# Kernel optimization log

Hardware: AMD Instinct MI355X
Metric: run time of the kernel (lower is better)

## Reference

```python
import jax, jax.numpy as jnp
import numpy as np

N_PRED = 2_000_000   # predicted reflections (incl. harmonics)
N_OBS = 1_000_000    # merged observations (harmonic groups)
RASU = 200_000       # reciprocal ASU size
N_IMAGES = 2000
HMAX = 60
GRID = 2 * HMAX + 1  # 121
MC = 32              # mc_samples
D_META = 5
KL_WEIGHT = 1.0
LOG2PI = float(np.log(2.0 * np.pi))

# 3 reindexing ops as integer 3x3 matrices: identity, inversion, a permutation op
OPS = np.stack([
    np.eye(3, dtype=np.int32),
    -np.eye(3, dtype=np.int32),
    np.array([[0, 1, 0], [1, 0, 0], [0, 0, -1]], dtype=np.int32),
])


def setup_inputs() -> dict:
    key = jax.random.key(0)
    ks = jax.random.split(key, 12)
    hkl = jax.random.randint(ks[0], (N_PRED, 3), -HMAX, HMAX + 1, dtype=jnp.int32)
    asu_table = jax.random.randint(ks[1], (GRID ** 3,), 0, RASU, dtype=jnp.int32)
    harmonic_id = jnp.arange(N_PRED, dtype=jnp.int32) // 2  # 2 harmonics per obs, max = N_OBS-1
    image_id = jax.random.randint(ks[2], (N_PRED,), 0, N_IMAGES, dtype=jnp.int32)
    I = jax.random.normal(ks[3], (N_OBS,), dtype=jnp.float32)
    SigI = jax.random.uniform(ks[4], (N_OBS,), minval=0.5, maxval=1.5, dtype=jnp.float32)
    metadata = jax.random.normal(ks[5], (N_PRED, D_META), dtype=jnp.float32)
    q_loc = jax.random.normal(ks[6], (RASU,), dtype=jnp.float32)
    q_raw_scale = jax.random.normal(ks[7], (RASU,), dtype=jnp.float32) * 0.1
    eps = jax.random.normal(ks[8], (MC, RASU), dtype=jnp.float32)
    scale_w = jax.random.normal(ks[9], (D_META + 4,), dtype=jnp.float32) * 0.01
    scale_b = jnp.zeros((), dtype=jnp.float32)
    image_bias = jax.random.normal(ks[10], (N_IMAGES,), dtype=jnp.float32) * 0.01
    return dict(hkl=hkl, I=I, SigI=SigI, image_id=image_id, metadata=metadata,
                harmonic_id=harmonic_id, asu_table=asu_table, q_loc=q_loc,
                q_raw_scale=q_raw_scale, eps=eps, scale_w=scale_w, scale_b=scale_b,
                image_bias=image_bias)


def reference(hkl, I, SigI, image_id, metadata, harmonic_id, asu_table,
              q_loc, q_raw_scale, eps, scale_w, scale_b, image_bias):
    q_scale = jax.nn.softplus(q_raw_scale) + 1e-6
    # KL(q || N(0,1)) for Normal q, then mean over reflections
    kl_div = jnp.mean(-jnp.log(q_scale) + 0.5 * (q_scale ** 2 + q_loc ** 2) - 0.5)

    Imodel = jnp.stack([q_loc, q_scale], axis=-1)           # [RASU, 2]
    Iscale = jnp.stack([I, SigI], axis=-1)[harmonic_id]      # [N_PRED, 2] (gathered per prediction)
    zT = (q_loc[None, :] + q_scale[None, :] * eps).T         # rsample -> [RASU, MC]

    log_sig = jnp.log(SigI)[:, None]
    lls = []
    for op in OPS:  # small fixed loop over reindexing ops
        _hkl = hkl @ jnp.asarray(op).T                       # [N_PRED, 3]
        flat = ((_hkl[:, 0] + HMAX) * GRID + (_hkl[:, 1] + HMAX)) * GRID + (_hkl[:, 2] + HMAX)
        refl_id = asu_table[flat]                            # reciprocal_asu lookup [N_PRED]
        feats = jnp.concatenate([Imodel[refl_id], Iscale, metadata], axis=-1)  # [N_PRED, 9]
        scale = jnp.exp(feats @ scale_w + scale_b + image_bias[image_id])[:, None]
        Ipred = zT[refl_id] * scale                          # [N_PRED, MC]
        # convolve: scatter-add harmonics into observations
        Ipred = jax.ops.segment_sum(Ipred, harmonic_id, num_segments=N_OBS)  # [N_OBS, MC]
        ll = -0.5 * ((Ipred - I[:, None]) / SigI[:, None]) ** 2 - log_sig - 0.5 * LOG2PI
        # build per-observation image id (default 1, overwritten by scatter)
        img_obs = jnp.ones((N_OBS,), jnp.int32).at[harmonic_id].set(image_id)
        ll = jax.ops.segment_sum(ll, img_obs, num_segments=N_IMAGES) / MC     # [N_IMAGES, MC]
        lls.append(ll.mean(-1))
    llcat = jnp.stack(lls, axis=-1)                          # [N_IMAGES, n_ops]
    op_idx = jnp.argmax(llcat, axis=-1)
    ll = jnp.mean(jnp.max(llcat, axis=-1))
    elbo = -ll + KL_WEIGHT * kl_div
    return elbo, op_idx
```

## Files before the change

kernel.cpp:

```cpp
#include <hip/hip_runtime.h>
#include <math.h>

#define N_PRED   2000000
#define N_OBS    1000000
#define RASU     200000
#define N_IMAGES 2000
#define HMAX     60
#define GRID_    121
#define NGRID3   1771561
#define NPAIRS   885781
#define MC       32
#define NPART    64
#define LOG2PI_D 1.8378770664093453
#define PREP_PAD 33

typedef float f4 __attribute__((ext_vector_type(4)));
typedef float f2 __attribute__((ext_vector_type(2)));
typedef int   i2 __attribute__((ext_vector_type(2)));

#define NTL(p) __builtin_nontemporal_load(p)

__global__ __launch_bounds__(256)
void repack_kernel(const int* __restrict__ asu, unsigned int* __restrict__ lo16w,
                   unsigned int* __restrict__ hi2, f4* __restrict__ zero_base,
                   int zero_count)
{
    __shared__ unsigned int hbits[256];
    int j = blockIdx.x * 256 + threadIdx.x;
    unsigned int myh = 0;
    if (j < NPAIRS) {
        int i0 = 2 * j;
        i2 a;
        if (i0 + 1 < NGRID3) a = *(const i2*)(asu + i0);
        else { a.x = asu[i0]; a.y = 0; }
        lo16w[j] = ((unsigned int)a.x & 0xFFFFu) | (((unsigned int)a.y & 0xFFFFu) << 16);
        myh = (((unsigned int)a.x >> 16) & 3u) | ((((unsigned int)a.y >> 16) & 3u) << 2);
    }
    hbits[threadIdx.x] = myh;
    __syncthreads();
    if ((threadIdx.x & 7) == 0 && j < NPAIRS) {
        unsigned int wbits = 0;
#pragma unroll
        for (int k = 0; k < 8; k++) wbits |= hbits[threadIdx.x + k] << (4 * k);
        hi2[j >> 3] = wbits;
    }
    f4 zero = {0.f, 0.f, 0.f, 0.f};
    for (int k = j; k < zero_count; k += gridDim.x * 256) zero_base[k] = zero;
}

__global__ __launch_bounds__(256)
void prep_kernel(const float* __restrict__ qloc, const float* __restrict__ qraw,
                 const float* __restrict__ eps, const float* __restrict__ sw,
                 float* __restrict__ Qs, float* __restrict__ ZS,
                 double* __restrict__ accums, int useZ)
{
    __shared__ float lds[256 * PREP_PAD];
    int t = threadIdx.x;
    int base = blockIdx.x * 256;
    int r = base + t;
    bool valid = (r < RASU);
    double klv = 0.0;
    float qs = 1.f, ql = 0.f, ewq = 0.f;
    if (valid) {
        float x  = qraw[r];
        float sp = (x > 0.f) ? (x + log1pf(expf(-x))) : log1pf(expf(x));
        qs = sp + 1e-6f;
        ql = qloc[r];
        Qs[r] = qs;
        ewq = expf(fmaf(sw[0], ql, sw[1] * qs));
        klv = (double)(-logf(qs) + 0.5f * (qs * qs + ql * ql) - 0.5f);
    }
#pragma unroll
    for (int off = 32; off; off >>= 1) klv += __shfl_down(klv, off);
    if ((t & 63) == 0) atomicAdd(&accums[0], klv);

    if (useZ) {
#pragma unroll 8
        for (int k = 0; k < MC; k++) {
            float v = valid ? fmaf(qs, eps[(size_t)k * RASU + r], ql) * ewq : 0.f;
            lds[t * PREP_PAD + k] = v;
        }
        __syncthreads();
        int rr0 = t >> 3, cc = t & 7;
        f4* Zp = (f4*)ZS;
#pragma unroll
        for (int i = 0; i < 8; i++) {
            int rr  = rr0 + i * 32;
            int row = base + rr;
            const float* p = &lds[rr * PREP_PAD + cc * 4];
            f4 v = {p[0], p[1], p[2], p[3]};
            if (row < RASU) Zp[(size_t)row * 8 + cc] = v;
        }
    }
}

template <int USEZ, int USELOHI>
__global__ __launch_bounds__(256)
void obs_kernel(const int* __restrict__ hkl, const float* __restrict__ I,
                const float* __restrict__ SigI, const int* __restrict__ image_id,
                const float* __restrict__ metadata, const int* __restrict__ asu,
                const unsigned short* __restrict__ lo16, const unsigned int* __restrict__ hi2,
                const float* __restrict__ qloc, const float* __restrict__ Qs,
                const float* __restrict__ ZS, const float* __restrict__ eps,
                const float* __restrict__ sw, const float* __restrict__ sbp,
                const float* __restrict__ ibias, double* __restrict__ partial)
{
    int o = blockIdx.x * 256 + threadIdx.x;
    if (o >= N_OBS) return;

    float w[9];
#pragma unroll
    for (int j = 0; j < 9; j++) w[j] = sw[j];
    float sb = sbp[0];

    float Iv = NTL(I + o), Sv = NTL(SigI + o);
    float inv  = 1.0f / Sv;
    float logs = logf(Sv);

    int p0 = 2 * o;
    i2 ia = NTL((const i2*)(image_id + p0));
    int img = ia.y;

    float eb[2];
    {
        const f2* m0 = (const f2*)(metadata + (size_t)p0 * 5);
        f2 ma = NTL(m0), mb = NTL(m0 + 1), mc_ = NTL(m0 + 2), md = NTL(m0 + 3), me = NTL(m0 + 4);
        float m[10] = {ma.x, ma.y, mb.x, mb.y, mc_.x, mc_.y, md.x, md.y, me.x, me.y};
#pragma unroll
        for (int j = 0; j < 2; j++) {
            float b = w[2] * Iv;
            b = fmaf(w[3], Sv, b);
#pragma unroll
            for (int k = 0; k < 5; k++) b = fmaf(w[4 + k], m[5 * j + k], b);
            eb[j] = expf(b + sb + ibias[j == 0 ? ia.x : ia.y]);
        }
    }

    int h[2][3];
    {
        const i2* hp = (const i2*)(hkl + (size_t)p0 * 3);
        i2 h01 = NTL(hp), h23 = NTL(hp + 1), h45 = NTL(hp + 2);
        h[0][0] = h01.x; h[0][1] = h01.y; h[0][2] = h23.x;
        h[1][0] = h23.y; h[1][1] = h45.x; h[1][2] = h45.y;
    }

    int r[3][2];
#pragma unroll
    for (int j = 0; j < 2; j++) {
        int flat[3];
        flat[0] = ((h[j][0] + HMAX) * GRID_ + (h[j][1] + HMAX)) * GRID_ + (h[j][2] + HMAX);
        flat[1] = (NGRID3 - 1) - flat[0];
        flat[2] = ((h[j][1] + HMAX) * GRID_ + (h[j][0] + HMAX)) * GRID_ + (HMAX - h[j][2]);
#pragma unroll
        for (int op = 0; op < 3; op++) {
            if (USELOHI) {
                int f = flat[op];
                int lo = (int)lo16[f];
                int hi = (int)((hi2[f >> 4] >> ((f & 15) * 2)) & 3u);
                r[op][j] = lo | (hi << 16);
            } else {
                r[op][j] = asu[flat[op]];
            }
        }
    }

    float s0 = eb[0], s1 = eb[1];
    float acc[3] = {0.f, 0.f, 0.f};
    if (USEZ) {
        const f4* Zp = (const f4*)ZS;
#pragma unroll
        for (int op = 0; op < 3; op++) {
            const f4* pa = Zp + (size_t)r[op][0] * 8;
            const f4* pb = Zp + (size_t)r[op][1] * 8;
            float a3 = 0.f;
#pragma unroll
            for (int c = 0; c < 8; c++) {
                f4 a = pa[c];
                f4 b = pb[c];
                float t;
                t = (fmaf(b.x, s1, a.x * s0) - Iv) * inv; a3 = fmaf(t, t, a3);
                t = (fmaf(b.y, s1, a.y * s0) - Iv) * inv; a3 = fmaf(t, t, a3);
                t = (fmaf(b.z, s1, a.z * s0) - Iv) * inv; a3 = fmaf(t, t, a3);
                t = (fmaf(b.w, s1, a.w * s0) - Iv) * inv; a3 = fmaf(t, t, a3);
            }
            acc[op] = a3;
        }
    } else {
#pragma unroll
        for (int op = 0; op < 3; op++) {
            float q0a = qloc[r[op][0]], q1a = Qs[r[op][0]];
            float q0b = qloc[r[op][1]], q1b = Qs[r[op][1]];
            float sa = s0 * expf(fmaf(w[0], q0a, w[1] * q1a));
            float sb2 = s1 * expf(fmaf(w[0], q0b, w[1] * q1b));
            float a3 = 0.f;
            for (int mc = 0; mc < MC; mc++) {
                const float* ep = eps + (size_t)mc * RASU;
                float z0 = fmaf(q1a, ep[r[op][0]], q0a);
                float z1 = fmaf(q1b, ep[r[op][1]], q0b);
                float t = (fmaf(z1, sb2, z0 * sa) - Iv) * inv;
                a3 = fmaf(t, t, a3);
            }
            acc[op] = a3;
        }
    }

    double base_ll = -32.0 * ((double)logs + 0.5 * LOG2PI_D);
    int pidx = (int)(blockIdx.x & (NPART - 1));
    double* pp = partial + ((size_t)pidx * N_IMAGES + img) * 3;
#pragma unroll
    for (int op = 0; op < 3; op++) {
        double ll = -0.5 * (double)acc[op] + base_ll;
        atomicAdd(pp + op, ll);
    }
}

__global__ __launch_bounds__(256)
void img_kernel(const double* __restrict__ partial, double* __restrict__ accums,
                float* __restrict__ out)
{
    int i = blockIdx.x * 256 + threadIdx.x;
    if (i >= N_IMAGES) return;
    double l0 = 0, l1 = 0, l2 = 0;
    for (int p = 0; p < NPART; p++) {
        const double* q = partial + ((size_t)p * N_IMAGES + i) * 3;
        l0 += q[0]; l1 += q[1]; l2 += q[2];
    }
    const double ninv = 1.0 / (double)(MC * MC);
    l0 *= ninv; l1 *= ninv; l2 *= ninv;
    int idx = 0; double best = l0;
    if (l1 > best) { best = l1; idx = 1; }
    if (l2 > best) { best = l2; idx = 2; }
    out[1 + i] = (float)idx;
    atomicAdd(&accums[1], best);
}

__global__ void final_kernel(const double* __restrict__ accums, float* __restrict__ out)
{
    double elbo = -(accums[1] / (double)N_IMAGES) + (accums[0] / (double)RASU);
    out[0] = (float)elbo;
}

extern "C" void kernel_launch(void* const* d_in, const int* in_sizes, int n_in,
                              void* d_out, int out_size, void* d_ws, size_t ws_size,
                              hipStream_t stream)
{
    const int*   hkl      = (const int*)  d_in[0];
    const float* I        = (const float*)d_in[1];
    const float* SigI     = (const float*)d_in[2];
    const int*   image_id = (const int*)  d_in[3];
    const float* metadata = (const float*)d_in[4];
    const int*   asu      = (const int*)  d_in[6];
    const float* qloc     = (const float*)d_in[7];
    const float* qraw     = (const float*)d_in[8];
    const float* eps      = (const float*)d_in[9];
    const float* sw       = (const float*)d_in[10];
    const float* sb       = (const float*)d_in[11];
    const float* ibias    = (const float*)d_in[12];
    float* out = (float*)d_out;

    char* ws = (char*)d_ws;
    size_t off = 0;
    double* partial = (double*)(ws + off); off += (size_t)NPART * N_IMAGES * 3 * sizeof(double);
    double* accums  = (double*)(ws + off); off += 2 * sizeof(double);
    off = (off + 15) & ~(size_t)15;
    float*  Qs      = (float*) (ws + off); off += (size_t)RASU * sizeof(float);
    unsigned int* lo16w = (unsigned int*)(ws + off); off += (size_t)NPAIRS * sizeof(unsigned int);
    unsigned int* hi2   = (unsigned int*)(ws + off); off += (size_t)((NPAIRS + 7) / 8) * sizeof(unsigned int);
    int useLoHi = (off <= ws_size) ? 1 : 0;
    off = (off + 127) & ~(size_t)127;
    float* ZS = (float*)(ws + off);
    size_t zbytes = (size_t)RASU * MC * sizeof(float);
    int useZ = (off + zbytes <= ws_size) ? 1 : 0;

    int zero_count = (int)((NPART * N_IMAGES * 3 * sizeof(double) + 2 * sizeof(double) + 15) / 16);
    int repackBlocks = (NPAIRS + 255) / 256;
    if (useLoHi) {
        repack_kernel<<<repackBlocks, 256, 0, stream>>>(asu, lo16w, hi2, (f4*)partial, zero_count);
    } else {
        (void)hipMemsetAsync(partial, 0, (size_t)zero_count * 16, stream);
    }

    prep_kernel<<<(RASU + 255) / 256, 256, 0, stream>>>(qloc, qraw, eps, sw, Qs, ZS, accums, useZ);

    int blocksC = (N_OBS + 255) / 256;
    const unsigned short* lo16 = (const unsigned short*)lo16w;
    if (useZ && useLoHi)
        obs_kernel<1,1><<<blocksC, 256, 0, stream>>>(hkl, I, SigI, image_id, metadata, asu, lo16, hi2,
                                                     qloc, Qs, ZS, eps, sw, sb, ibias, partial);
    else if (useZ)
        obs_kernel<1,0><<<blocksC, 256, 0, stream>>>(hkl, I, SigI, image_id, metadata, asu, lo16, hi2,
                                                     qloc, Qs, ZS, eps, sw, sb, ibias, partial);
    else if (useLoHi)
        obs_kernel<0,1><<<blocksC, 256, 0, stream>>>(hkl, I, SigI, image_id, metadata, asu, lo16, hi2,
                                                     qloc, Qs, ZS, eps, sw, sb, ibias, partial);
    else
        obs_kernel<0,0><<<blocksC, 256, 0, stream>>>(hkl, I, SigI, image_id, metadata, asu, lo16, hi2,
                                                     qloc, Qs, ZS, eps, sw, sb, ibias, partial);

    img_kernel<<<(N_IMAGES + 255) / 256, 256, 0, stream>>>(partial, accums, out);
    final_kernel<<<1, 1, 0, stream>>>(accums, out);
}
```

Baseline: 466.8 us.

## Cooperatively gather Z rows with 8 lanes per observation via wave shuffles

Restructures the Z-table gather so that each observation's six 128-byte rows are read by 8 cooperating lanes (one f4 each) instead of one thread reading 8 consecutive f4s per row. Per-observation indices and scalars are broadcast with __shfl, partial sums are reduced with xor shuffles, and one lane issues the atomics. This aims to turn scattered per-thread strided loads into coalesced row reads and to cut outstanding memory requests per lane. In exchange it adds many shuffles and a loop over 8 observations per wave.

```diff
diff --git a/kernel.cpp b/kernel.cpp
--- a/kernel.cpp
+++ b/kernel.cpp
@@ -94,6 +94,16 @@
     }
 }
 
+__device__ __forceinline__ float tsum4(f4 a, f4 b, float s0, float s1, float Iv, float inv)
+{
+    float acc = 0.f, t;
+    t = (fmaf(b.x, s1, a.x * s0) - Iv) * inv; acc = fmaf(t, t, acc);
+    t = (fmaf(b.y, s1, a.y * s0) - Iv) * inv; acc = fmaf(t, t, acc);
+    t = (fmaf(b.z, s1, a.z * s0) - Iv) * inv; acc = fmaf(t, t, acc);
+    t = (fmaf(b.w, s1, a.w * s0) - Iv) * inv; acc = fmaf(t, t, acc);
+    return acc;
+}
+
 template <int USEZ, int USELOHI>
 __global__ __launch_bounds__(256)
 void obs_kernel(const int* __restrict__ hkl, const float* __restrict__ I,
@@ -105,112 +115,135 @@
                 const float* __restrict__ sw, const float* __restrict__ sbp,
                 const float* __restrict__ ibias, double* __restrict__ partial)
 {
-    int o = blockIdx.x * 256 + threadIdx.x;
-    if (o >= N_OBS) return;
+    int tid  = threadIdx.x;
+    int lane = tid & 63;
+    int o = blockIdx.x * 256 + tid;
+    bool valid = (o < N_OBS);
 
     float w[9];
 #pragma unroll
     for (int j = 0; j < 9; j++) w[j] = sw[j];
-    float sb = sbp[0];
-
-    float Iv = NTL(I + o), Sv = NTL(SigI + o);
-    float inv  = 1.0f / Sv;
-    float logs = logf(Sv);
-
-    int p0 = 2 * o;
-    i2 ia = NTL((const i2*)(image_id + p0));
-    int img = ia.y;
-
-    float eb[2];
-    {
+    float sbv = sbp[0];
+
+    float Iv = 0.f, Sv = 1.f;
+    int img = -1;
+    float eb0 = 0.f, eb1 = 0.f;
+    int r00 = 0, r01 = 0, r10 = 0, r11 = 0, r20 = 0, r21 = 0;
+
+    if (valid) {
+        Iv = NTL(I + o); Sv = NTL(SigI + o);
+        int p0 = 2 * o;
+        i2 ia = NTL((const i2*)(image_id + p0));
+        img = ia.y;
+
         const f2* m0 = (const f2*)(metadata + (size_t)p0 * 5);
         f2 ma = NTL(m0), mb = NTL(m0 + 1), mc_ = NTL(m0 + 2), md = NTL(m0 + 3), me = NTL(m0 + 4);
         float m[10] = {ma.x, ma.y, mb.x, mb.y, mc_.x, mc_.y, md.x, md.y, me.x, me.y};
+        float eb[2];
 #pragma unroll
         for (int j = 0; j < 2; j++) {
             float b = w[2] * Iv;
             b = fmaf(w[3], Sv, b);
 #pragma unroll
             for (int k = 0; k < 5; k++) b = fmaf(w[4 + k], m[5 * j + k], b);
-            eb[j] = expf(b + sb + ibias[j == 0 ? ia.x : ia.y]);
-        }
-    }
-
-    int h[2][3];
-    {
+            eb[j] = expf(b + sbv + ibias[j == 0 ? ia.x : ia.y]);
+        }
+        eb0 = eb[0]; eb1 = eb[1];
+
+        int h[2][3];
         const i2* hp = (const i2*)(hkl + (size_t)p0 * 3);
         i2 h01 = NTL(hp), h23 = NTL(hp + 1), h45 = NTL(hp + 2);
         h[0][0] = h01.x; h[0][1] = h01.y; h[0][2] = h23.x;
         h[1][0] = h23.y; h[1][1] = h45.x; h[1][2] = h45.y;
-    }
-
-    int r[3][2];
-#pragma unroll
-    for (int j = 0; j < 2; j++) {
-        int flat[3];
-        flat[0] = ((h[j][0] + HMAX) * GRID_ + (h[j][1] + HMAX)) * GRID_ + (h[j][2] + HMAX);
-        flat[1] = (NGRID3 - 1) - flat[0];
-        flat[2] = ((h[j][1] + HMAX) * GRID_ + (h[j][0] + HMAX)) * GRID_ + (HMAX - h[j][2]);
-#pragma unroll
-        for (int op = 0; op < 3; op++) {
-            if (USELOHI) {
-                int f = flat[op];
-                int lo = (int)lo16[f];
-                int hi = (int)((hi2[f >> 4] >> ((f & 15) * 2)) & 3u);
-                r[op][j] = lo | (hi << 16);
-            } else {
-                r[op][j] = asu[flat[op]];
+
+        int r[3][2];
+#pragma unroll
+        for (int j = 0; j < 2; j++) {
+            int flat[3];
+            flat[0] = ((h[j][0] + HMAX) * GRID_ + (h[j][1] + HMAX)) * GRID_ + (h[j][2] + HMAX);
+            flat[1] = (NGRID3 - 1) - flat[0];
+            flat[2] = ((h[j][1] + HMAX) * GRID_ + (h[j][0] + HMAX)) * GRID_ + (HMAX - h[j][2]);
+#pragma unroll
+            for (int op = 0; op < 3; op++) {
+                if (USELOHI) {
+                    int f = flat[op];
+                    int lo = (int)lo16[f];
+                    int hi = (int)((hi2[f >> 4] >> ((f & 15) * 2)) & 3u);
+                    r[op][j] = lo | (hi << 16);
+                } else {
+                    r[op][j] = asu[flat[op]];
+                }
             }
         }
-    }
-
-    float s0 = eb[0], s1 = eb[1];
-    float acc[3] = {0.f, 0.f, 0.f};
+        r00 = r[0][0]; r01 = r[0][1];
+        r10 = r[1][0]; r11 = r[1][1];
+        r20 = r[2][0]; r21 = r[2][1];
+    }
+
+    float inv  = 1.0f / Sv;
+    float logs = logf(Sv);
+    int pidx = (int)(blockIdx.x & (NPART - 1));
+
     if (USEZ) {
         const f4* Zp = (const f4*)ZS;
+        int grp = lane >> 3, sub = lane & 7;
+#pragma unroll
+        for (int i = 0; i < 8; i++) {
+            int L = i * 8 + grp;
+            int   im = __shfl(img, L, 64);
+            int  q00 = __shfl(r00, L, 64), q01 = __shfl(r01, L, 64);
+            int  q10 = __shfl(r10, L, 64), q11 = __shfl(r11, L, 64);
+            int  q20 = __shfl(r20, L, 64), q21 = __shfl(r21, L, 64);
+            float S0 = __shfl(eb0, L, 64), S1 = __shfl(eb1, L, 64);
+            float CI = __shfl(Iv,  L, 64), CV = __shfl(inv, L, 64);
+            float LG = __shfl(logs, L, 64);
+            if (im >= 0) {
+                f4 A0 = Zp[(size_t)q00 * 8 + sub], B0 = Zp[(size_t)q01 * 8 + sub];
+                f4 A1 = Zp[(size_t)q10 * 8 + sub], B1 = Zp[(size_t)q11 * 8 + sub];
+                f4 A2 = Zp[(size_t)q20 * 8 + sub], B2 = Zp[(size_t)q21 * 8 + sub];
+                float a0 = tsum4(A0, B0, S0, S1, CI, CV);
+                float a1 = tsum4(A1, B1, S0, S1, CI, CV);
+                float a2 = tsum4(A2, B2, S0, S1, CI, CV);
+#pragma unroll
+                for (int msk = 1; msk <= 4; msk <<= 1) {
+                    a0 += __shfl_xor(a0, msk, 64);
+                    a1 += __shfl_xor(a1, msk, 64);
+                    a2 += __shfl_xor(a2, msk, 64);
+                }
+                if (sub == 0) {
+                    double base_ll = -32.0 * ((double)LG + 0.5 * LOG2PI_D);
+                    double* pp = partial + ((size_t)pidx * N_IMAGES + im) * 3;
+                    atomicAdd(pp + 0, -0.5 * (double)a0 + base_ll);
+                    atomicAdd(pp + 1, -0.5 * (double)a1 + base_ll);
+                    atomicAdd(pp + 2, -0.5 * (double)a2 + base_ll);
+                }
+            }
+        }
+    } else {
+        if (!valid) return;
+        int rr[3][2] = {{r00, r01}, {r10, r11}, {r20, r21}};
+        float acc[3];
 #pragma unroll
         for (int op = 0; op < 3; op++) {
-            const f4* pa = Zp + (size_t)r[op][0] * 8;
-            const f4* pb = Zp + (size_t)r[op][1] * 8;
-            float a3 = 0.f;
-#pragma unroll
-            for (int c = 0; c < 8; c++) {
-                f4 a = pa[c];
-                f4 b = pb[c];
-                float t;
-                t = (fmaf(b.x, s1, a.x * s0) - Iv) * inv; a3 = fmaf(t, t, a3);
-                t = (fmaf(b.y, s1, a.y * s0) - Iv) * inv; a3 = fmaf(t, t, a3);
-                t = (fmaf(b.z, s1, a.z * s0) - Iv) * inv; a3 = fmaf(t, t, a3);
-                t = (fmaf(b.w, s1, a.w * s0) - Iv) * inv; a3 = fmaf(t, t, a3);
-            }
-            acc[op] = a3;
-        }
-    } else {
-#pragma unroll
-        for (int op = 0; op < 3; op++) {
-            float q0a = qloc[r[op][0]], q1a = Qs[r[op][0]];
-            float q0b = qloc[r[op][1]], q1b = Qs[r[op][1]];
-            float sa = s0 * expf(fmaf(w[0], q0a, w[1] * q1a));
-            float sb2 = s1 * expf(fmaf(w[0], q0b, w[1] * q1b));
+            float q0a = qloc[rr[op][0]], q1a = Qs[rr[op][0]];
+            float q0b = qloc[rr[op][1]], q1b = Qs[rr[op][1]];
+            float sa  = eb0 * expf(fmaf(w[0], q0a, w[1] * q1a));
+            float sb2 = eb1 * expf(fmaf(w[0], q0b, w[1] * q1b));
             float a3 = 0.f;
             for (int mc = 0; mc < MC; mc++) {
                 const float* ep = eps + (size_t)mc * RASU;
-                float z0 = fmaf(q1a, ep[r[op][0]], q0a);
-                float z1 = fmaf(q1b, ep[r[op][1]], q0b);
+                float z0 = fmaf(q1a, ep[rr[op][0]], q0a);
+                float z1 = fmaf(q1b, ep[rr[op][1]], q0b);
                 float t = (fmaf(z1, sb2, z0 * sa) - Iv) * inv;
                 a3 = fmaf(t, t, a3);
             }
             acc[op] = a3;
         }
-    }
-
-    double base_ll = -32.0 * ((double)logs + 0.5 * LOG2PI_D);
-    int pidx = (int)(blockIdx.x & (NPART - 1));
-    double* pp = partial + ((size_t)pidx * N_IMAGES + img) * 3;
-#pragma unroll
-    for (int op = 0; op < 3; op++) {
-        double ll = -0.5 * (double)acc[op] + base_ll;
-        atomicAdd(pp + op, ll);
+        double base_ll = -32.0 * ((double)logs + 0.5 * LOG2PI_D);
+        double* pp = partial + ((size_t)pidx * N_IMAGES + img) * 3;
+#pragma unroll
+        for (int op = 0; op < 3; op++)
+            atomicAdd(pp + op, -0.5 * (double)acc[op] + base_ll);
     }
 }
 
```

Measured after the change: 394.2 us. -15.5%, faster.
